# Kernel tuning notes

Measured on AMD Instinct MI355X. Metric: run time of the kernel, lower is better.

Reference implementation:

```python
import jax, jax.numpy as jnp
import numpy as np

B, L, H, W, C = 2, 5, 48, 176, 256
HEADS, DIM_HEAD = 8, 32
INNER = HEADS * DIM_HEAD  # 256
SCALE = DIM_HEAD ** -0.5


def setup_inputs() -> dict:
    key = jax.random.key(0)
    k1, k2, k3, k4, k5 = jax.random.split(key, 5)
    x = jax.random.normal(k1, (B, L, H, W, C), dtype=jnp.float32)
    # mask of shape (B, H, W, 1, L); slot 0 always valid so no softmax row is fully masked
    mask = jax.random.randint(k2, (B, H, W, 1, L), 0, 2, dtype=jnp.int32)
    mask = mask.at[..., 0].set(1)
    w_qkv = jax.random.normal(k3, (C, 3 * INNER), dtype=jnp.float32) / np.sqrt(C)
    w_out = jax.random.normal(k4, (INNER, C), dtype=jnp.float32) / np.sqrt(INNER)
    b_out = jax.random.normal(k5, (C,), dtype=jnp.float32) * 0.01
    return {"x": x, "mask": mask, "w_qkv": w_qkv, "w_out": w_out, "b_out": b_out}


def reference(x, mask, w_qkv, w_out, b_out):
    # x: (B, L, H, W, C) -> (B, H, W, L, C)
    xp = jnp.transpose(x, (0, 2, 3, 1, 4))
    qkv = xp @ w_qkv  # (B, H, W, L, 3*INNER)
    q, k, v = jnp.split(qkv, 3, axis=-1)
    # split heads: (B, H, W, L, M, D)
    shp = (B, H, W, L, HEADS, DIM_HEAD)
    q = q.reshape(shp)
    k = k.reshape(shp)
    v = v.reshape(shp)
    # attention over the small CAV axis L
    att = jnp.einsum('bhwimd,bhwjmd->bmhwij', q, k) * SCALE  # (B,M,H,W,L,L)
    m = mask[:, None]  # (B,1,H,W,1,L) broadcasts over (B,M,H,W,i,j)
    att = jnp.where(m == 0, -jnp.inf, att)
    att = jax.nn.softmax(att, axis=-1)
    out = jnp.einsum('bmhwij,bhwjmd->bhwimd', att, v)  # (B,H,W,L,M,D)
    out = out.reshape(B, H, W, L, INNER)
    out = out @ w_out + b_out  # dropout is identity in eval
    return jnp.transpose(out, (0, 3, 1, 2, 4))  # (B, L, H, W, C)
```

## Files before the change

kernel.cpp:

```cpp
#include <hip/hip_runtime.h>


typedef __attribute__((ext_vector_type(8))) short short8;
typedef __attribute__((ext_vector_type(4))) float f32x4;

#define M_ALL 84480
#define SCALE_F 0.17677669529663687f

__device__ __forceinline__ float b2f(unsigned short u) {
    union { unsigned u; float f; } x; x.u = ((unsigned)u) << 16; return x.f;
}
__device__ __forceinline__ unsigned short f2b(float f) {
    union { float f; unsigned u; } x; x.f = f;
    unsigned u = x.u;
    return (unsigned short)((u + 0x7FFFu + ((u >> 16) & 1u)) >> 16);
}

__device__ __forceinline__ size_t row_to_xoff(int r) {
    int l = r % 5; int t = r / 5;
    int w = t % 176; t /= 176;
    int h = t % 48; int b = t / 48;
    return (size_t)(((b * 5 + l) * 48 + h) * 176 + w) * 256;
}

__global__ __launch_bounds__(256) void k_prep(const float* __restrict__ wq,
                                              const float* __restrict__ wo,
                                              unsigned short* __restrict__ wqt,
                                              unsigned short* __restrict__ wot) {
    int i = blockIdx.x * 256 + threadIdx.x;
    if (i < 196608) { int k = i / 768, n = i % 768; wqt[n * 256 + k] = f2b(wq[i]); }
    if (i < 65536)  { int k = i / 256, n = i % 256; wot[n * 256 + k] = f2b(wo[i]); }
}

__global__ __launch_bounds__(256) void k_qkv(const float* __restrict__ x,
                                             const unsigned short* __restrict__ wqt,
                                             unsigned short* __restrict__ qkv) {
    __shared__ unsigned short As[64 * 264];
    __shared__ unsigned short Bs[64 * 136];
    const int tid = threadIdx.x;
    const int m0 = blockIdx.x * 64;

#pragma unroll
    for (int rep = 0; rep < 16; ++rep) {
        int e = rep * 1024 + tid * 4;
        int row = e >> 8, k = e & 255;
        size_t xo = row_to_xoff(m0 + row) + k;
        float4 v = *(const float4*)(x + xo);
        ushort4 o; o.x = f2b(v.x); o.y = f2b(v.y); o.z = f2b(v.z); o.w = f2b(v.w);
        *(ushort4*)&As[row * 264 + k] = o;
    }

    const int wv = tid >> 6, lane = tid & 63;
    const int ln = lane & 15, quad = lane >> 4;
    const int m_w = (wv >> 1) * 32, n_w = (wv & 1) * 32;

    for (int nc = 0; nc < 12; ++nc) {
        const int n0 = nc * 64;
        f32x4 acc[2][2];
#pragma unroll
        for (int i = 0; i < 2; ++i)
#pragma unroll
            for (int j = 0; j < 2; ++j) acc[i][j] = (f32x4){0.f, 0.f, 0.f, 0.f};

        for (int kh = 0; kh < 2; ++kh) {
            __syncthreads();
#pragma unroll
            for (int rep = 0; rep < 4; ++rep) {
                int flat = rep * 2048 + tid * 8;
                int nl = flat >> 7;
                int kl = flat & 127;
                const unsigned short* src = wqt + (size_t)(n0 + nl) * 256 + kh * 128 + kl;
                ushort4 p0 = *(const ushort4*)(src);
                ushort4 p1 = *(const ushort4*)(src + 4);
                *(ushort4*)&Bs[nl * 136 + kl] = p0;
                *(ushort4*)&Bs[nl * 136 + kl + 4] = p1;
            }
            __syncthreads();
#pragma unroll
            for (int kk = 0; kk < 4; ++kk) {
                int ka = kh * 128 + kk * 32 + quad * 8;
                int kb = kk * 32 + quad * 8;
                short8 a0 = *(const short8*)&As[(m_w + ln) * 264 + ka];
                short8 a1 = *(const short8*)&As[(m_w + 16 + ln) * 264 + ka];
                short8 b0 = *(const short8*)&Bs[(n_w + ln) * 136 + kb];
                short8 b1 = *(const short8*)&Bs[(n_w + 16 + ln) * 136 + kb];
                acc[0][0] = __builtin_amdgcn_mfma_f32_16x16x32_bf16(a0, b0, acc[0][0], 0, 0, 0);
                acc[0][1] = __builtin_amdgcn_mfma_f32_16x16x32_bf16(a0, b1, acc[0][1], 0, 0, 0);
                acc[1][0] = __builtin_amdgcn_mfma_f32_16x16x32_bf16(a1, b0, acc[1][0], 0, 0, 0);
                acc[1][1] = __builtin_amdgcn_mfma_f32_16x16x32_bf16(a1, b1, acc[1][1], 0, 0, 0);
            }
        }
#pragma unroll
        for (int i = 0; i < 2; ++i)
#pragma unroll
            for (int j = 0; j < 2; ++j) {
                int row = m0 + m_w + 16 * i + quad * 4;
                int col = n0 + n_w + 16 * j + ln;
#pragma unroll
                for (int rg = 0; rg < 4; ++rg)
                    qkv[(size_t)(row + rg) * 768 + col] = f2b(acc[i][j][rg]);
            }
    }
}

__global__ __launch_bounds__(64) void k_attn(const unsigned short* __restrict__ qkv,
                                             const int* __restrict__ mask,
                                             unsigned short* __restrict__ att) {
    const int p = blockIdx.x;
    const int g = threadIdx.x >> 3;
    const int l8 = threadIdx.x & 7;
    const size_t base = (size_t)p * 3840 + g * 32 + l8 * 4;

    float q[5][4], k[5][4], v[5][4];
#pragma unroll
    for (int i = 0; i < 5; ++i) {
        ushort4 uq = *(const ushort4*)(qkv + base + i * 768);
        ushort4 uk = *(const ushort4*)(qkv + base + i * 768 + 256);
        ushort4 uv = *(const ushort4*)(qkv + base + i * 768 + 512);
        q[i][0] = b2f(uq.x); q[i][1] = b2f(uq.y); q[i][2] = b2f(uq.z); q[i][3] = b2f(uq.w);
        k[i][0] = b2f(uk.x); k[i][1] = b2f(uk.y); k[i][2] = b2f(uk.z); k[i][3] = b2f(uk.w);
        v[i][0] = b2f(uv.x); v[i][1] = b2f(uv.y); v[i][2] = b2f(uv.z); v[i][3] = b2f(uv.w);
    }

    float s[5][5];
#pragma unroll
    for (int i = 0; i < 5; ++i)
#pragma unroll
        for (int j = 0; j < 5; ++j)
            s[i][j] = q[i][0] * k[j][0] + q[i][1] * k[j][1] + q[i][2] * k[j][2] + q[i][3] * k[j][3];
#pragma unroll
    for (int off = 4; off >= 1; off >>= 1)
#pragma unroll
        for (int i = 0; i < 5; ++i)
#pragma unroll
            for (int j = 0; j < 5; ++j) s[i][j] += __shfl_xor(s[i][j], off, 64);

    int mk[5];
#pragma unroll
    for (int j = 0; j < 5; ++j) mk[j] = mask[p * 5 + j];

    float pr[5][5];
#pragma unroll
    for (int i = 0; i < 5; ++i) {
        float mx = -1e30f;
#pragma unroll
        for (int j = 0; j < 5; ++j) {
            s[i][j] = mk[j] ? s[i][j] * SCALE_F : -1e30f;
            mx = fmaxf(mx, s[i][j]);
        }
        float sum = 0.f;
#pragma unroll
        for (int j = 0; j < 5; ++j) { pr[i][j] = __expf(s[i][j] - mx); sum += pr[i][j]; }
        float inv = 1.f / sum;
#pragma unroll
        for (int j = 0; j < 5; ++j) pr[i][j] *= inv;
    }

#pragma unroll
    for (int i = 0; i < 5; ++i) {
        float o0 = 0.f, o1 = 0.f, o2 = 0.f, o3 = 0.f;
#pragma unroll
        for (int j = 0; j < 5; ++j) {
            o0 += pr[i][j] * v[j][0]; o1 += pr[i][j] * v[j][1];
            o2 += pr[i][j] * v[j][2]; o3 += pr[i][j] * v[j][3];
        }
        ushort4 u; u.x = f2b(o0); u.y = f2b(o1); u.z = f2b(o2); u.w = f2b(o3);
        *(ushort4*)(att + (size_t)(p * 5 + i) * 256 + g * 32 + l8 * 4) = u;
    }
}

__global__ __launch_bounds__(256) void k_out(const unsigned short* __restrict__ att,
                                             const unsigned short* __restrict__ wot,
                                             const float* __restrict__ bo,
                                             float* __restrict__ out) {
    __shared__ unsigned short As[64 * 264];
    __shared__ unsigned short Bs[64 * 136];
    const int tid = threadIdx.x;
    const int m0 = blockIdx.x * 64;

#pragma unroll
    for (int rep = 0; rep < 8; ++rep) {
        int flat = rep * 2048 + tid * 8;
        int row = flat >> 8;
        int k = flat & 255;
        const unsigned short* src = att + (size_t)(m0 + row) * 256 + k;
        ushort4 p0 = *(const ushort4*)(src);
        ushort4 p1 = *(const ushort4*)(src + 4);
        *(ushort4*)&As[row * 264 + k] = p0;
        *(ushort4*)&As[row * 264 + k + 4] = p1;
    }

    const int wv = tid >> 6, lane = tid & 63;
    const int ln = lane & 15, quad = lane >> 4;
    const int m_w = (wv >> 1) * 32, n_w = (wv & 1) * 32;

    for (int nc = 0; nc < 4; ++nc) {
        const int n0 = nc * 64;
        f32x4 acc[2][2];
#pragma unroll
        for (int i = 0; i < 2; ++i)
#pragma unroll
            for (int j = 0; j < 2; ++j) acc[i][j] = (f32x4){0.f, 0.f, 0.f, 0.f};

        for (int kh = 0; kh < 2; ++kh) {
            __syncthreads();
#pragma unroll
            for (int rep = 0; rep < 4; ++rep) {
                int flat = rep * 2048 + tid * 8;
                int nl = flat >> 7;
                int kl = flat & 127;
                const unsigned short* src = wot + (size_t)(n0 + nl) * 256 + kh * 128 + kl;
                ushort4 p0 = *(const ushort4*)(src);
                ushort4 p1 = *(const ushort4*)(src + 4);
                *(ushort4*)&Bs[nl * 136 + kl] = p0;
                *(ushort4*)&Bs[nl * 136 + kl + 4] = p1;
            }
            __syncthreads();
#pragma unroll
            for (int kk = 0; kk < 4; ++kk) {
                int ka = kh * 128 + kk * 32 + quad * 8;
                int kb = kk * 32 + quad * 8;
                short8 a0 = *(const short8*)&As[(m_w + ln) * 264 + ka];
                short8 a1 = *(const short8*)&As[(m_w + 16 + ln) * 264 + ka];
                short8 b0 = *(const short8*)&Bs[(n_w + ln) * 136 + kb];
                short8 b1 = *(const short8*)&Bs[(n_w + 16 + ln) * 136 + kb];
                acc[0][0] = __builtin_amdgcn_mfma_f32_16x16x32_bf16(a0, b0, acc[0][0], 0, 0, 0);
                acc[0][1] = __builtin_amdgcn_mfma_f32_16x16x32_bf16(a0, b1, acc[0][1], 0, 0, 0);
                acc[1][0] = __builtin_amdgcn_mfma_f32_16x16x32_bf16(a1, b0, acc[1][0], 0, 0, 0);
                acc[1][1] = __builtin_amdgcn_mfma_f32_16x16x32_bf16(a1, b1, acc[1][1], 0, 0, 0);
            }
        }
        float bv0 = bo[n0 + n_w + ln];
        float bv1 = bo[n0 + n_w + 16 + ln];
#pragma unroll
        for (int i = 0; i < 2; ++i)
#pragma unroll
            for (int rg = 0; rg < 4; ++rg) {
                int r = m0 + m_w + 16 * i + quad * 4 + rg;
                size_t off = row_to_xoff(r);
                out[off + n0 + n_w + ln] = acc[i][0][rg] + bv0;
                out[off + n0 + n_w + 16 + ln] = acc[i][1][rg] + bv1;
            }
    }
}

extern "C" void kernel_launch(void* const* d_in, const int* in_sizes, int n_in,
                              void* d_out, int out_size, void* d_ws, size_t ws_size,
                              hipStream_t stream) {
    const float* x   = (const float*)d_in[0];
    const int* mask  = (const int*)d_in[1];
    const float* wq  = (const float*)d_in[2];
    const float* wo  = (const float*)d_in[3];
    const float* bo  = (const float*)d_in[4];
    float* out = (float*)d_out;

    char* ws = (char*)d_ws;
    unsigned short* qkv = (unsigned short*)(ws);
    unsigned short* att = (unsigned short*)(ws + 129761280);
    unsigned short* wqt = (unsigned short*)(ws + 173015040);
    unsigned short* wot = (unsigned short*)(ws + 173408256);

    hipLaunchKernelGGL(k_prep, dim3(768), dim3(256), 0, stream, wq, wo, wqt, wot);
    hipLaunchKernelGGL(k_qkv, dim3(1320), dim3(256), 0, stream, x, wqt, qkv);
    hipLaunchKernelGGL(k_attn, dim3(16896), dim3(64), 0, stream, qkv, mask, att);
    hipLaunchKernelGGL(k_out, dim3(1320), dim3(256), 0, stream, att, wot, bo, out);
}
```

Before: 280.8 us.

## Fuse QKV projection with attention and read weights directly from global

```diff
diff --git a/kernel.cpp b/kernel.cpp
--- a/kernel.cpp
+++ b/kernel.cpp
@@ -4,7 +4,6 @@
 typedef __attribute__((ext_vector_type(8))) short short8;
 typedef __attribute__((ext_vector_type(4))) float f32x4;
 
-#define M_ALL 84480
 #define SCALE_F 0.17677669529663687f
 
 __device__ __forceinline__ float b2f(unsigned short u) {
@@ -21,6 +20,10 @@
     int w = t % 176; t /= 176;
     int h = t % 48; int b = t / 48;
     return (size_t)(((b * 5 + l) * 48 + h) * 176 + w) * 256;
+}
+
+__device__ __forceinline__ int lidx(int r, int c) {
+    return r * 256 + ((((c >> 3) ^ (r & 7)) << 3) | (c & 7));
 }
 
 __global__ __launch_bounds__(256) void k_prep(const float* __restrict__ wq,
@@ -32,112 +35,122 @@
     if (i < 65536)  { int k = i / 256, n = i % 256; wot[n * 256 + k] = f2b(wo[i]); }
 }
 
-__global__ __launch_bounds__(256) void k_qkv(const float* __restrict__ x,
-                                             const unsigned short* __restrict__ wqt,
-                                             unsigned short* __restrict__ qkv) {
-    __shared__ unsigned short As[64 * 264];
-    __shared__ unsigned short Bs[64 * 136];
+__device__ __forceinline__ void qkv_pass(const unsigned short* __restrict__ xs,
+                                         unsigned short* __restrict__ dst,
+                                         const unsigned short* __restrict__ wrow,
+                                         int n0w, int ln, int quad) {
+    f32x4 acc[3][4];
+#pragma unroll
+    for (int m = 0; m < 3; ++m)
+#pragma unroll
+        for (int n = 0; n < 4; ++n) acc[m][n] = (f32x4){0.f, 0.f, 0.f, 0.f};
+
+#pragma unroll
+    for (int kk = 0; kk < 8; ++kk) {
+        short8 a[3], b[4];
+#pragma unroll
+        for (int m = 0; m < 3; ++m) {
+            int row = m * 16 + ln;
+            if (row < 40)
+                a[m] = *(const short8*)&xs[lidx(row, kk * 32 + quad * 8)];
+            else
+                a[m] = (short8){0, 0, 0, 0, 0, 0, 0, 0};
+        }
+#pragma unroll
+        for (int n = 0; n < 4; ++n)
+            b[n] = *(const short8*)&wrow[(size_t)(n0w + n * 16 + ln) * 256 + kk * 32 + quad * 8];
+#pragma unroll
+        for (int m = 0; m < 3; ++m)
+#pragma unroll
+            for (int n = 0; n < 4; ++n)
+                acc[m][n] = __builtin_amdgcn_mfma_f32_16x16x32_bf16(a[m], b[n], acc[m][n], 0, 0, 0);
+    }
+#pragma unroll
+    for (int m = 0; m < 3; ++m)
+#pragma unroll
+        for (int n = 0; n < 4; ++n)
+#pragma unroll
+            for (int rg = 0; rg < 4; ++rg) {
+                int row = m * 16 + quad * 4 + rg;
+                if (row < 40) {
+                    int col = n0w + n * 16 + ln;
+                    dst[lidx(row, col)] = f2b(acc[m][n][rg]);
+                }
+            }
+}
+
+__global__ __launch_bounds__(256) void k_qkv_attn(const float* __restrict__ x,
+                                                  const unsigned short* __restrict__ wqt,
+                                                  const int* __restrict__ mask,
+                                                  unsigned short* __restrict__ att) {
+    __shared__ unsigned short xs[40 * 256];
+    __shared__ unsigned short qs[40 * 256];
+    __shared__ unsigned short kvs[40 * 256];
     const int tid = threadIdx.x;
-    const int m0 = blockIdx.x * 64;
-
-#pragma unroll
-    for (int rep = 0; rep < 16; ++rep) {
-        int e = rep * 1024 + tid * 4;
-        int row = e >> 8, k = e & 255;
-        size_t xo = row_to_xoff(m0 + row) + k;
-        float4 v = *(const float4*)(x + xo);
-        ushort4 o; o.x = f2b(v.x); o.y = f2b(v.y); o.z = f2b(v.z); o.w = f2b(v.w);
-        *(ushort4*)&As[row * 264 + k] = o;
-    }
+    const int blk = blockIdx.x;
+    const int rbase = blk * 40;
+
+#pragma unroll
+    for (int i = 0; i < 5; ++i) {
+        int u = i * 256 + tid;
+        int r = u >> 5, cb = u & 31;
+        size_t xo = row_to_xoff(rbase + r) + cb * 8;
+        float4 v0 = *(const float4*)(x + xo);
+        float4 v1 = *(const float4*)(x + xo + 4);
+        short8 o;
+        o[0] = (short)f2b(v0.x); o[1] = (short)f2b(v0.y);
+        o[2] = (short)f2b(v0.z); o[3] = (short)f2b(v0.w);
+        o[4] = (short)f2b(v1.x); o[5] = (short)f2b(v1.y);
+        o[6] = (short)f2b(v1.z); o[7] = (short)f2b(v1.w);
+        *(short8*)&xs[lidx(r, cb * 8)] = o;
+    }
+    __syncthreads();
 
     const int wv = tid >> 6, lane = tid & 63;
     const int ln = lane & 15, quad = lane >> 4;
-    const int m_w = (wv >> 1) * 32, n_w = (wv & 1) * 32;
-
-    for (int nc = 0; nc < 12; ++nc) {
-        const int n0 = nc * 64;
-        f32x4 acc[2][2];
-#pragma unroll
-        for (int i = 0; i < 2; ++i)
-#pragma unroll
-            for (int j = 0; j < 2; ++j) acc[i][j] = (f32x4){0.f, 0.f, 0.f, 0.f};
-
-        for (int kh = 0; kh < 2; ++kh) {
-            __syncthreads();
-#pragma unroll
-            for (int rep = 0; rep < 4; ++rep) {
-                int flat = rep * 2048 + tid * 8;
-                int nl = flat >> 7;
-                int kl = flat & 127;
-                const unsigned short* src = wqt + (size_t)(n0 + nl) * 256 + kh * 128 + kl;
-                ushort4 p0 = *(const ushort4*)(src);
-                ushort4 p1 = *(const ushort4*)(src + 4);
-                *(ushort4*)&Bs[nl * 136 + kl] = p0;
-                *(ushort4*)&Bs[nl * 136 + kl + 4] = p1;
-            }
-            __syncthreads();
-#pragma unroll
-            for (int kk = 0; kk < 4; ++kk) {
-                int ka = kh * 128 + kk * 32 + quad * 8;
-                int kb = kk * 32 + quad * 8;
-                short8 a0 = *(const short8*)&As[(m_w + ln) * 264 + ka];
-                short8 a1 = *(const short8*)&As[(m_w + 16 + ln) * 264 + ka];
-                short8 b0 = *(const short8*)&Bs[(n_w + ln) * 136 + kb];
-                short8 b1 = *(const short8*)&Bs[(n_w + 16 + ln) * 136 + kb];
-                acc[0][0] = __builtin_amdgcn_mfma_f32_16x16x32_bf16(a0, b0, acc[0][0], 0, 0, 0);
-                acc[0][1] = __builtin_amdgcn_mfma_f32_16x16x32_bf16(a0, b1, acc[0][1], 0, 0, 0);
-                acc[1][0] = __builtin_amdgcn_mfma_f32_16x16x32_bf16(a1, b0, acc[1][0], 0, 0, 0);
-                acc[1][1] = __builtin_amdgcn_mfma_f32_16x16x32_bf16(a1, b1, acc[1][1], 0, 0, 0);
-            }
-        }
-#pragma unroll
-        for (int i = 0; i < 2; ++i)
-#pragma unroll
-            for (int j = 0; j < 2; ++j) {
-                int row = m0 + m_w + 16 * i + quad * 4;
-                int col = n0 + n_w + 16 * j + ln;
-#pragma unroll
-                for (int rg = 0; rg < 4; ++rg)
-                    qkv[(size_t)(row + rg) * 768 + col] = f2b(acc[i][j][rg]);
-            }
-    }
-}
-
-__global__ __launch_bounds__(64) void k_attn(const unsigned short* __restrict__ qkv,
-                                             const int* __restrict__ mask,
-                                             unsigned short* __restrict__ att) {
-    const int p = blockIdx.x;
-    const int g = threadIdx.x >> 3;
-    const int l8 = threadIdx.x & 7;
-    const size_t base = (size_t)p * 3840 + g * 32 + l8 * 4;
-
-    float q[5][4], k[5][4], v[5][4];
-#pragma unroll
-    for (int i = 0; i < 5; ++i) {
-        ushort4 uq = *(const ushort4*)(qkv + base + i * 768);
-        ushort4 uk = *(const ushort4*)(qkv + base + i * 768 + 256);
-        ushort4 uv = *(const ushort4*)(qkv + base + i * 768 + 512);
-        q[i][0] = b2f(uq.x); q[i][1] = b2f(uq.y); q[i][2] = b2f(uq.z); q[i][3] = b2f(uq.w);
-        k[i][0] = b2f(uk.x); k[i][1] = b2f(uk.y); k[i][2] = b2f(uk.z); k[i][3] = b2f(uk.w);
-        v[i][0] = b2f(uv.x); v[i][1] = b2f(uv.y); v[i][2] = b2f(uv.z); v[i][3] = b2f(uv.w);
-    }
-
+    const int n0w = wv * 64;
+
+    qkv_pass(xs, qs, wqt, n0w, ln, quad);
+    qkv_pass(xs, kvs, wqt + 256 * 256, n0w, ln, quad);
+    __syncthreads();
+
+    const int p_l = tid >> 2, part = tid & 3;
+    const int g = p_l >> 3, h = p_l & 7;
+    const int c0 = h * 32 + part * 8;
+
+    float qf[5][8];
+#pragma unroll
+    for (int i = 0; i < 5; ++i) {
+        short8 qv = *(const short8*)&qs[lidx(g * 5 + i, c0)];
+#pragma unroll
+        for (int d = 0; d < 8; ++d) qf[i][d] = b2f((unsigned short)qv[d]);
+    }
     float s[5][5];
 #pragma unroll
+    for (int j = 0; j < 5; ++j) {
+        short8 kv = *(const short8*)&kvs[lidx(g * 5 + j, c0)];
+        float kf[8];
+#pragma unroll
+        for (int d = 0; d < 8; ++d) kf[d] = b2f((unsigned short)kv[d]);
+#pragma unroll
+        for (int i = 0; i < 5; ++i) {
+            float acc = 0.f;
+#pragma unroll
+            for (int d = 0; d < 8; ++d) acc += qf[i][d] * kf[d];
+            s[i][j] = acc;
+        }
+    }
+#pragma unroll
     for (int i = 0; i < 5; ++i)
 #pragma unroll
-        for (int j = 0; j < 5; ++j)
-            s[i][j] = q[i][0] * k[j][0] + q[i][1] * k[j][1] + q[i][2] * k[j][2] + q[i][3] * k[j][3];
-#pragma unroll
-    for (int off = 4; off >= 1; off >>= 1)
-#pragma unroll
-        for (int i = 0; i < 5; ++i)
-#pragma unroll
-            for (int j = 0; j < 5; ++j) s[i][j] += __shfl_xor(s[i][j], off, 64);
+        for (int j = 0; j < 5; ++j) {
+            s[i][j] += __shfl_xor(s[i][j], 1, 64);
+            s[i][j] += __shfl_xor(s[i][j], 2, 64);
+        }
 
     int mk[5];
 #pragma unroll
-    for (int j = 0; j < 5; ++j) mk[j] = mask[p * 5 + j];
+    for (int j = 0; j < 5; ++j) mk[j] = mask[(blk * 8 + g) * 5 + j];
 
     float pr[5][5];
 #pragma unroll
@@ -155,17 +168,33 @@
 #pragma unroll
         for (int j = 0; j < 5; ++j) pr[i][j] *= inv;
     }
-
-#pragma unroll
-    for (int i = 0; i < 5; ++i) {
-        float o0 = 0.f, o1 = 0.f, o2 = 0.f, o3 = 0.f;
-#pragma unroll
-        for (int j = 0; j < 5; ++j) {
-            o0 += pr[i][j] * v[j][0]; o1 += pr[i][j] * v[j][1];
-            o2 += pr[i][j] * v[j][2]; o3 += pr[i][j] * v[j][3];
-        }
-        ushort4 u; u.x = f2b(o0); u.y = f2b(o1); u.z = f2b(o2); u.w = f2b(o3);
-        *(ushort4*)(att + (size_t)(p * 5 + i) * 256 + g * 32 + l8 * 4) = u;
+    __syncthreads();
+
+    qkv_pass(xs, kvs, wqt + 512 * 256, n0w, ln, quad);
+    __syncthreads();
+
+    float o[5][8];
+#pragma unroll
+    for (int i = 0; i < 5; ++i)
+#pragma unroll
+        for (int d = 0; d < 8; ++d) o[i][d] = 0.f;
+#pragma unroll
+    for (int j = 0; j < 5; ++j) {
+        short8 vv = *(const short8*)&kvs[lidx(g * 5 + j, c0)];
+        float vf[8];
+#pragma unroll
+        for (int d = 0; d < 8; ++d) vf[d] = b2f((unsigned short)vv[d]);
+#pragma unroll
+        for (int i = 0; i < 5; ++i)
+#pragma unroll
+            for (int d = 0; d < 8; ++d) o[i][d] += pr[i][j] * vf[d];
+    }
+#pragma unroll
+    for (int i = 0; i < 5; ++i) {
+        short8 ov;
+#pragma unroll
+        for (int d = 0; d < 8; ++d) ov[d] = (short)f2b(o[i][d]);
+        *(short8*)(att + (size_t)(rbase + g * 5 + i) * 256 + c0) = ov;
     }
 }
 
@@ -174,74 +203,57 @@
                                              const float* __restrict__ bo,
                                              float* __restrict__ out) {
     __shared__ unsigned short As[64 * 264];
-    __shared__ unsigned short Bs[64 * 136];
     const int tid = threadIdx.x;
     const int m0 = blockIdx.x * 64;
 
 #pragma unroll
-    for (int rep = 0; rep < 8; ++rep) {
-        int flat = rep * 2048 + tid * 8;
-        int row = flat >> 8;
-        int k = flat & 255;
-        const unsigned short* src = att + (size_t)(m0 + row) * 256 + k;
-        ushort4 p0 = *(const ushort4*)(src);
-        ushort4 p1 = *(const ushort4*)(src + 4);
-        *(ushort4*)&As[row * 264 + k] = p0;
-        *(ushort4*)&As[row * 264 + k + 4] = p1;
-    }
+    for (int i = 0; i < 8; ++i) {
+        int u = i * 256 + tid;
+        int r = u >> 5, cb = u & 31;
+        *(short8*)&As[r * 264 + cb * 8] =
+            *(const short8*)&att[(size_t)(m0 + r) * 256 + cb * 8];
+    }
+    __syncthreads();
 
     const int wv = tid >> 6, lane = tid & 63;
     const int ln = lane & 15, quad = lane >> 4;
-    const int m_w = (wv >> 1) * 32, n_w = (wv & 1) * 32;
-
-    for (int nc = 0; nc < 4; ++nc) {
-        const int n0 = nc * 64;
-        f32x4 acc[2][2];
-#pragma unroll
-        for (int i = 0; i < 2; ++i)
-#pragma unroll
-            for (int j = 0; j < 2; ++j) acc[i][j] = (f32x4){0.f, 0.f, 0.f, 0.f};
-
-        for (int kh = 0; kh < 2; ++kh) {
-            __syncthreads();
-#pragma unroll
-            for (int rep = 0; rep < 4; ++rep) {
-                int flat = rep * 2048 + tid * 8;
-                int nl = flat >> 7;
-                int kl = flat & 127;
-                const unsigned short* src = wot + (size_t)(n0 + nl) * 256 + kh * 128 + kl;
-                ushort4 p0 = *(const ushort4*)(src);
-                ushort4 p1 = *(const ushort4*)(src + 4);
-                *(ushort4*)&Bs[nl * 136 + kl] = p0;
-                *(ushort4*)&Bs[nl * 136 + kl + 4] = p1;
-            }
-            __syncthreads();
-#pragma unroll
-            for (int kk = 0; kk < 4; ++kk) {
-                int ka = kh * 128 + kk * 32 + quad * 8;
-                int kb = kk * 32 + quad * 8;
-                short8 a0 = *(const short8*)&As[(m_w + ln) * 264 + ka];
-                short8 a1 = *(const short8*)&As[(m_w + 16 + ln) * 264 + ka];
-                short8 b0 = *(const short8*)&Bs[(n_w + ln) * 136 + kb];
-                short8 b1 = *(const short8*)&Bs[(n_w + 16 + ln) * 136 + kb];
-                acc[0][0] = __builtin_amdgcn_mfma_f32_16x16x32_bf16(a0, b0, acc[0][0], 0, 0, 0);
-                acc[0][1] = __builtin_amdgcn_mfma_f32_16x16x32_bf16(a0, b1, acc[0][1], 0, 0, 0);
-                acc[1][0] = __builtin_amdgcn_mfma_f32_16x16x32_bf16(a1, b0, acc[1][0], 0, 0, 0);
-                acc[1][1] = __builtin_amdgcn_mfma_f32_16x16x32_bf16(a1, b1, acc[1][1], 0, 0, 0);
-            }
-        }
-        float bv0 = bo[n0 + n_w + ln];
-        float bv1 = bo[n0 + n_w + 16 + ln];
-#pragma unroll
-        for (int i = 0; i < 2; ++i)
-#pragma unroll
-            for (int rg = 0; rg < 4; ++rg) {
-                int r = m0 + m_w + 16 * i + quad * 4 + rg;
-                size_t off = row_to_xoff(r);
-                out[off + n0 + n_w + ln] = acc[i][0][rg] + bv0;
-                out[off + n0 + n_w + 16 + ln] = acc[i][1][rg] + bv1;
-            }
-    }
+    const int n0w = wv * 64;
+
+    f32x4 acc[4][4];
+#pragma unroll
+    for (int m = 0; m < 4; ++m)
+#pragma unroll
+        for (int n = 0; n < 4; ++n) acc[m][n] = (f32x4){0.f, 0.f, 0.f, 0.f};
+
+#pragma unroll
+    for (int kk = 0; kk < 8; ++kk) {
+        short8 a[4], b[4];
+#pragma unroll
+        for (int m = 0; m < 4; ++m)
+            a[m] = *(const short8*)&As[(m * 16 + ln) * 264 + kk * 32 + quad * 8];
+#pragma unroll
+        for (int n = 0; n < 4; ++n)
+            b[n] = *(const short8*)&wot[(size_t)(n0w + n * 16 + ln) * 256 + kk * 32 + quad * 8];
+#pragma unroll
+        for (int m = 0; m < 4; ++m)
+#pragma unroll
+            for (int n = 0; n < 4; ++n)
+                acc[m][n] = __builtin_amdgcn_mfma_f32_16x16x32_bf16(a[m], b[n], acc[m][n], 0, 0, 0);
+    }
+
+    float bv[4];
+#pragma unroll
+    for (int n = 0; n < 4; ++n) bv[n] = bo[n0w + n * 16 + ln];
+#pragma unroll
+    for (int m = 0; m < 4; ++m)
+#pragma unroll
+        for (int rg = 0; rg < 4; ++rg) {
+            int r = m0 + m * 16 + quad * 4 + rg;
+            size_t off = row_to_xoff(r);
+#pragma unroll
+            for (int n = 0; n < 4; ++n)
+                out[off + n0w + n * 16 + ln] = acc[m][n][rg] + bv[n];
+        }
 }
 
 extern "C" void kernel_launch(void* const* d_in, const int* in_sizes, int n_in,
@@ -255,13 +267,11 @@
     float* out = (float*)d_out;
 
     char* ws = (char*)d_ws;
-    unsigned short* qkv = (unsigned short*)(ws);
-    unsigned short* att = (unsigned short*)(ws + 129761280);
-    unsigned short* wqt = (unsigned short*)(ws + 173015040);
-    unsigned short* wot = (unsigned short*)(ws + 173408256);
+    unsigned short* att = (unsigned short*)(ws);
+    unsigned short* wqt = (unsigned short*)(ws + 43253760);
+    unsigned short* wot = (unsigned short*)(ws + 43253760 + 393216);
 
     hipLaunchKernelGGL(k_prep, dim3(768), dim3(256), 0, stream, wq, wo, wqt, wot);
-    hipLaunchKernelGGL(k_qkv, dim3(1320), dim3(256), 0, stream, x, wqt, qkv);
-    hipLaunchKernelGGL(k_attn, dim3(16896), dim3(64), 0, stream, qkv, mask, att);
+    hipLaunchKernelGGL(k_qkv_attn, dim3(2112), dim3(256), 0, stream, x, wqt, mask, att);
     hipLaunchKernelGGL(k_out, dim3(1320), dim3(256), 0, stream, att, wot, bo, out);
 }
```

Result: slower. 334.4 us (+19.1%).
